# Kernel optimization log

Measured on AMD Instinct MI355X. Metric: run time of the kernel, lower is better.

Reference implementation:

```python
import jax, jax.numpy as jnp
import numpy as np

NUM_HEADS = 16
TOP_K = 6


def setup_inputs() -> dict:
    key = jax.random.key(0)
    ks = jax.random.split(key, 16)
    B, P = 8192, 4096
    QD = PD = D = 1024  # query_dim, prototype_dim, token_dim
    s = lambda d: 1.0 / np.sqrt(d)
    return {
        "query": jax.random.normal(ks[0], (B, QD), jnp.float32),
        "prototype_bank": jax.random.normal(ks[1], (P, PD), jnp.float32),
        "prototype_logits": jax.random.normal(ks[2], (B, P), jnp.float32),
        # query_proj / prototype_proj (torch Linear: y = x @ W.T + b)
        "Wq_proj": jax.random.normal(ks[3], (D, QD), jnp.float32) * s(QD),
        "bq_proj": jnp.zeros((D,), jnp.float32),
        "Wp_proj": jax.random.normal(ks[4], (D, PD), jnp.float32) * s(PD),
        "bp_proj": jnp.zeros((D,), jnp.float32),
        # MultiheadAttention in-proj (q, k, v) and out-proj
        "Wq": jax.random.normal(ks[5], (D, D), jnp.float32) * s(D),
        "bq": jnp.zeros((D,), jnp.float32),
        "Wk": jax.random.normal(ks[6], (D, D), jnp.float32) * s(D),
        "bk": jnp.zeros((D,), jnp.float32),
        "Wv": jax.random.normal(ks[7], (D, D), jnp.float32) * s(D),
        "bv": jnp.zeros((D,), jnp.float32),
        "Wo": jax.random.normal(ks[8], (D, D), jnp.float32) * s(D),
        "bo": jnp.zeros((D,), jnp.float32),
    }


def reference(query, prototype_bank, prototype_logits,
              Wq_proj, bq_proj, Wp_proj, bp_proj,
              Wq, bq, Wk, bk, Wv, bv, Wo, bo):
    B, D = query.shape[0], Wq.shape[0]
    h = NUM_HEADS
    dh = D // h
    k = min(TOP_K, prototype_bank.shape[0])

    # top-k prototype selection (indices only)
    _, topk_idx = jax.lax.top_k(prototype_logits, k)            # [B, k]

    projected_bank = prototype_bank @ Wp_proj.T + bp_proj        # [P, D]
    selected = projected_bank[topk_idx]                          # [B, k, D]

    attn_query = (query @ Wq_proj.T + bq_proj)[:, None, :]       # [B, 1, D]

    # MultiheadAttention (batch_first, eval mode so dropout is a no-op)
    qh = (attn_query @ Wq.T + bq).reshape(B, 1, h, dh).transpose(0, 2, 1, 3)  # [B,h,1,dh]
    kh = (selected @ Wk.T + bk).reshape(B, k, h, dh).transpose(0, 2, 1, 3)    # [B,h,k,dh]
    vh = (selected @ Wv.T + bv).reshape(B, k, h, dh).transpose(0, 2, 1, 3)    # [B,h,k,dh]

    scores = jnp.einsum("bhqd,bhkd->bhqk", qh, kh) / jnp.sqrt(jnp.float32(dh))
    w = jax.nn.softmax(scores, axis=-1)                          # [B,h,1,k]
    ctx = jnp.einsum("bhqk,bhkd->bhqd", w, vh)                   # [B,h,1,dh]
    ctx = ctx.transpose(0, 2, 1, 3).reshape(B, 1, D)
    context = ctx @ Wo.T + bo                                    # [B,1,D]

    attn_weights = w.mean(axis=1)                                # avg heads -> [B,1,k]
    return context[:, 0, :], attn_weights[:, 0, :]
```

## Files before the change

kernel.cpp:

```cpp
#include <hip/hip_runtime.h>
#include <stdint.h>

#define B_ROWS 8192
#define P_ROWS 4096
#define D_DIM  1024
#define K_TOP  6

typedef __attribute__((ext_vector_type(8))) short short8;
typedef __attribute__((ext_vector_type(4))) float floatx4;

static __device__ __forceinline__ float bf2f(unsigned short h) {
  return __uint_as_float(((unsigned)h) << 16);
}
static __device__ __forceinline__ unsigned short f2bf(float f) {
  unsigned u = __float_as_uint(f);
  u += 0x7FFFu + ((u >> 16) & 1u);
  return (unsigned short)(u >> 16);
}

struct ConvArgs {
  const float* s[8];
  unsigned short* d[8];
};
#define SEG0_END  8388608u
#define SEG1_END 12582912u
#define CONV_TOTAL 18874368u

__global__ __launch_bounds__(256) void convert_all_kernel(ConvArgs a) {
  unsigned e = (blockIdx.x * 256u + threadIdx.x) * 4u;
  int seg; unsigned base;
  if (e < SEG0_END) { seg = 0; base = 0; }
  else if (e < SEG1_END) { seg = 1; base = SEG0_END; }
  else {
    unsigned w = e - SEG1_END;
    seg = 2 + (int)(w >> 20);
    base = SEG1_END + (((unsigned)(seg - 2)) << 20);
  }
  unsigned off = e - base;
  float4 v = *(const float4*)(a.s[seg] + off);
  ushort4 o;
  o.x = f2bf(v.x); o.y = f2bf(v.y); o.z = f2bf(v.z); o.w = f2bf(v.w);
  *(ushort4*)(a.d[seg] + off) = o;
}

static __device__ __forceinline__ void cswap64(unsigned long long& hi, unsigned long long& lo) {
  unsigned long long a = hi, b = lo;
  bool c = b > a;
  hi = c ? b : a;
  lo = c ? a : b;
}

__global__ __launch_bounds__(256) void topk6_kernel(const float* __restrict__ logits,
                                                    int* __restrict__ out) {
  const int wid = threadIdx.x >> 6;
  const int lane = threadIdx.x & 63;
  const int row = blockIdx.x * 4 + wid;
  const float4* lp4 = (const float4*)(logits + (size_t)row * P_ROWS);

  unsigned long long m0 = 0, m1 = 0, m2 = 0, m3 = 0, m4 = 0, m5 = 0;

  auto ins = [&](float val, int idx) {
    unsigned u = __float_as_uint(val);
    u ^= ((unsigned)((int)u >> 31)) | 0x80000000u;
    unsigned long long key =
        (((unsigned long long)u) << 32) | (unsigned long long)(0xFFFFFFFFu - (unsigned)idx);
    m5 = key > m5 ? key : m5;
    cswap64(m4, m5);
    cswap64(m3, m4);
    cswap64(m2, m3);
    cswap64(m1, m2);
    cswap64(m0, m1);
  };

#pragma unroll
  for (int j = 0; j < 16; ++j) {
    float4 v = lp4[j * 64 + lane];
    const int base = j * 256 + lane * 4;
    ins(v.x, base);
    ins(v.y, base + 1);
    ins(v.z, base + 2);
    ins(v.w, base + 3);
  }

#pragma unroll
  for (int it = 0; it < K_TOP; ++it) {
    unsigned long long best = m0;
#pragma unroll
    for (int o = 32; o > 0; o >>= 1) {
      unsigned long long t = __shfl_xor(best, o);
      best = t > best ? t : best;
    }
    if (lane == 0)
      out[row * K_TOP + it] = (int)(0xFFFFFFFFu - (unsigned)(best & 0xFFFFFFFFull));
    const bool pred = (m0 == best);
    m0 = pred ? m1 : m0;
    m1 = pred ? m2 : m1;
    m2 = pred ? m3 : m2;
    m3 = pred ? m4 : m3;
    m4 = pred ? m5 : m4;
    m5 = pred ? 0ull : m5;
  }
}

typedef __attribute__((address_space(3))) unsigned int lds32_t;
typedef const __attribute__((address_space(1))) unsigned int g32_t;

static __device__ __forceinline__ void gld_lds16(const unsigned short* g, unsigned short* l) {
  __builtin_amdgcn_global_load_lds((g32_t*)(uintptr_t)g,
                                   (lds32_t*)(unsigned int)(uintptr_t)l, 16, 0, 0);
}

template <bool OUT_BF16>
static __device__ __forceinline__ void gemm_bt_body(
    const unsigned short* __restrict__ A, const unsigned short* __restrict__ Bw,
    const float* __restrict__ bias, void* __restrict__ Cout, int m0, int n0) {
  constexpr int Kd = 1024, Nd = 1024, BK = 64;
  __shared__ unsigned short sA[128 * BK];
  __shared__ unsigned short sB[128 * BK];

  const int tid = threadIdx.x;
  const int wid = tid >> 6, lane = tid & 63;
  const int wm = (wid & 1) * 64, wn = (wid >> 1) * 64;

  floatx4 acc[4][4];
#pragma unroll
  for (int mt = 0; mt < 4; ++mt)
#pragma unroll
    for (int nt = 0; nt < 4; ++nt) acc[mt][nt] = (floatx4){0.f, 0.f, 0.f, 0.f};

  const int ld_row = lane >> 3;
  const int ld_col = (lane & 7) * 8;

  for (int kt = 0; kt < Kd / BK; ++kt) {
    const int k0 = kt * BK;
    __syncthreads();
#pragma unroll
    for (int c = 0; c < 4; ++c) {
      const int ch = wid * 4 + c;
      const int r = ch * 8 + ld_row;
      gld_lds16(A  + (size_t)(m0 + r) * Kd + k0 + ld_col, sA + ch * 512);
      gld_lds16(Bw + (size_t)(n0 + r) * Kd + k0 + ld_col, sB + ch * 512);
    }
    __syncthreads();
#pragma unroll
    for (int ks = 0; ks < 2; ++ks) {
      const int kk = ks * 32 + (lane >> 4) * 8;
      short8 a[4], b[4];
#pragma unroll
      for (int t = 0; t < 4; ++t) {
        a[t] = *(const short8*)(sA + (wm + t * 16 + (lane & 15)) * BK + kk);
        b[t] = *(const short8*)(sB + (wn + t * 16 + (lane & 15)) * BK + kk);
      }
#pragma unroll
      for (int mt = 0; mt < 4; ++mt)
#pragma unroll
        for (int nt = 0; nt < 4; ++nt)
          acc[mt][nt] = __builtin_amdgcn_mfma_f32_16x16x32_bf16(a[mt], b[nt], acc[mt][nt], 0, 0, 0);
    }
  }

  const int er = lane >> 4;
  const int ec = lane & 15;
#pragma unroll
  for (int mt = 0; mt < 4; ++mt) {
#pragma unroll
    for (int nt = 0; nt < 4; ++nt) {
      const int col = n0 + wn + nt * 16 + ec;
      const float bv = bias[col];
#pragma unroll
      for (int r = 0; r < 4; ++r) {
        const int row = m0 + wm + mt * 16 + er * 4 + r;
        const float v = acc[mt][nt][r] + bv;
        if (OUT_BF16)
          ((unsigned short*)Cout)[(size_t)row * Nd + col] = f2bf(v);
        else
          ((float*)Cout)[(size_t)row * Nd + col] = v;
      }
    }
  }
}

template <bool OUT_BF16>
__global__ __launch_bounds__(256) void gemm_bt_kernel(
    const unsigned short* __restrict__ A, const unsigned short* __restrict__ Bw,
    const float* __restrict__ bias, void* __restrict__ Cout) {
  gemm_bt_body<OUT_BF16>(A, Bw, bias, Cout, blockIdx.y * 128, blockIdx.x * 128);
}

__global__ __launch_bounds__(256) void gemm_bt_dual_kernel(
    const unsigned short* __restrict__ A,
    const unsigned short* __restrict__ W0, const float* __restrict__ b0, unsigned short* C0,
    const unsigned short* __restrict__ W1, const float* __restrict__ b1, unsigned short* C1) {
  const unsigned short* Bw = blockIdx.z ? W1 : W0;
  const float* bias = blockIdx.z ? b1 : b0;
  unsigned short* C = blockIdx.z ? C1 : C0;
  gemm_bt_body<true>(A, Bw, bias, (void*)C, blockIdx.y * 128, blockIdx.x * 128);
}

__global__ __launch_bounds__(256) void attn_kernel(
    const unsigned short* __restrict__ q2,
    const unsigned short* __restrict__ kb,
    const unsigned short* __restrict__ vb,
    const int* __restrict__ topk,
    unsigned short* __restrict__ ctx,
    float* __restrict__ attnw) {
  const int b = blockIdx.x;
  const int wid = threadIdx.x >> 6, lane = threadIdx.x & 63;
  __shared__ float wsum[4][K_TOP];

  int idx[K_TOP];
#pragma unroll
  for (int j = 0; j < K_TOP; ++j) idx[j] = topk[b * K_TOP + j];

  float hw[K_TOP] = {0.f, 0.f, 0.f, 0.f, 0.f, 0.f};
#pragma unroll
  for (int hh = 0; hh < 4; ++hh) {
    const int h = wid * 4 + hh;
    const int off = h * 64 + lane;
    const float qv = bf2f(q2[(size_t)b * D_DIM + off]);
    float s[K_TOP];
#pragma unroll
    for (int j = 0; j < K_TOP; ++j)
      s[j] = qv * bf2f(kb[(size_t)idx[j] * D_DIM + off]);
#pragma unroll
    for (int j = 0; j < K_TOP; ++j)
#pragma unroll
      for (int o = 32; o > 0; o >>= 1) s[j] += __shfl_xor(s[j], o);

    float mx = -1e30f;
#pragma unroll
    for (int j = 0; j < K_TOP; ++j) mx = fmaxf(mx, s[j] * 0.125f);
    float e[K_TOP], sum = 0.f;
#pragma unroll
    for (int j = 0; j < K_TOP; ++j) { e[j] = __expf(s[j] * 0.125f - mx); sum += e[j]; }
    const float inv = 1.0f / sum;

    float o = 0.f;
#pragma unroll
    for (int j = 0; j < K_TOP; ++j) {
      const float w = e[j] * inv;
      hw[j] += w;
      o += w * bf2f(vb[(size_t)idx[j] * D_DIM + off]);
    }
    ctx[(size_t)b * D_DIM + off] = f2bf(o);
  }
  if (lane == 0) {
#pragma unroll
    for (int j = 0; j < K_TOP; ++j) wsum[wid][j] = hw[j];
  }
  __syncthreads();
  if (threadIdx.x < K_TOP) {
    const float t = wsum[0][threadIdx.x] + wsum[1][threadIdx.x] +
                    wsum[2][threadIdx.x] + wsum[3][threadIdx.x];
    attnw[(size_t)b * K_TOP + threadIdx.x] = t * (1.0f / 16.0f);
  }
}

extern "C" void kernel_launch(void* const* d_in, const int* in_sizes, int n_in,
                              void* d_out, int out_size, void* d_ws, size_t ws_size,
                              hipStream_t stream) {
  const float* query   = (const float*)d_in[0];
  const float* bank    = (const float*)d_in[1];
  const float* logits  = (const float*)d_in[2];
  const float* Wq_proj = (const float*)d_in[3];
  const float* bq_proj = (const float*)d_in[4];
  const float* Wp_proj = (const float*)d_in[5];
  const float* bp_proj = (const float*)d_in[6];
  const float* Wq      = (const float*)d_in[7];
  const float* bq      = (const float*)d_in[8];
  const float* Wk      = (const float*)d_in[9];
  const float* bk      = (const float*)d_in[10];
  const float* Wv      = (const float*)d_in[11];
  const float* bv      = (const float*)d_in[12];
  const float* Wo      = (const float*)d_in[13];
  const float* bo      = (const float*)d_in[14];

  char* ws = (char*)d_ws;
  size_t off = 0;
  auto alloc = [&](size_t bytes) {
    void* p = ws + off;
    off += (bytes + 255) & ~(size_t)255;
    return p;
  };
  unsigned short* q_bf    = (unsigned short*)alloc((size_t)B_ROWS * D_DIM * 2);
  unsigned short* bank_bf = (unsigned short*)alloc((size_t)P_ROWS * D_DIM * 2);
  unsigned short* q1_bf   = (unsigned short*)alloc((size_t)B_ROWS * D_DIM * 2);
  unsigned short* pb_bf   = (unsigned short*)alloc((size_t)P_ROWS * D_DIM * 2);
  unsigned short* vb_bf   = (unsigned short*)alloc((size_t)P_ROWS * D_DIM * 2);
  unsigned short* wqp_bf  = (unsigned short*)alloc((size_t)D_DIM * D_DIM * 2);
  unsigned short* wpp_bf  = (unsigned short*)alloc((size_t)D_DIM * D_DIM * 2);
  unsigned short* wq_bf   = (unsigned short*)alloc((size_t)D_DIM * D_DIM * 2);
  unsigned short* wk_bf   = (unsigned short*)alloc((size_t)D_DIM * D_DIM * 2);
  unsigned short* wv_bf   = (unsigned short*)alloc((size_t)D_DIM * D_DIM * 2);
  unsigned short* wo_bf   = (unsigned short*)alloc((size_t)D_DIM * D_DIM * 2);
  int* topk               = (int*)alloc((size_t)B_ROWS * K_TOP * 4);

  float* out_ctx  = (float*)d_out;
  float* out_attn = out_ctx + (size_t)B_ROWS * D_DIM;

  ConvArgs ca;
  ca.s[0] = query;   ca.d[0] = q_bf;
  ca.s[1] = bank;    ca.d[1] = bank_bf;
  ca.s[2] = Wq_proj; ca.d[2] = wqp_bf;
  ca.s[3] = Wp_proj; ca.d[3] = wpp_bf;
  ca.s[4] = Wq;      ca.d[4] = wq_bf;
  ca.s[5] = Wk;      ca.d[5] = wk_bf;
  ca.s[6] = Wv;      ca.d[6] = wv_bf;
  ca.s[7] = Wo;      ca.d[7] = wo_bf;
  convert_all_kernel<<<CONV_TOTAL / 1024, 256, 0, stream>>>(ca);

  topk6_kernel<<<B_ROWS / 4, 256, 0, stream>>>(logits, topk);

  auto gemm_bf = [&](const unsigned short* A, const unsigned short* W, const float* bias,
                     unsigned short* C, int M) {
    dim3 grid(D_DIM / 128, M / 128);
    gemm_bt_kernel<true><<<grid, 256, 0, stream>>>(A, W, bias, (void*)C);
  };
  gemm_bf(q_bf,    wqp_bf, bq_proj, q1_bf, B_ROWS);
  gemm_bf(bank_bf, wpp_bf, bp_proj, pb_bf, P_ROWS);
  gemm_bf(q1_bf,   wq_bf,  bq,      q_bf,  B_ROWS);

  {
    dim3 grid(D_DIM / 128, P_ROWS / 128, 2);
    gemm_bt_dual_kernel<<<grid, 256, 0, stream>>>(pb_bf, wk_bf, bk, bank_bf, wv_bf, bv, vb_bf);
  }

  attn_kernel<<<B_ROWS, 256, 0, stream>>>(q_bf, bank_bf, vb_bf, topk, q1_bf, out_attn);

  dim3 grid2(D_DIM / 128, B_ROWS / 128);
  gemm_bt_kernel<false><<<grid2, 256, 0, stream>>>(q1_bf, wo_bf, bo, d_out);
}
```

Before: 478.2 us.

## Fold input projections into attention in-projection weights to drop two GEMMs

Precomputes combined weights Wq·Wq_proj, Wk·Wp_proj and Wv·Wp_proj, plus the matching folded biases, using a small transpose and a batched 1024^3 GEMM. The query path then needs a single 8192x1024x1024 GEMM instead of two, and the bank path goes straight from the raw bank to K/V, dropping the intermediate projection GEMM. This removes roughly 12 GFLOP of large-GEMM work in exchange for about 3 GFLOP of weight-combining work on every call. The combined weights are rounded to bf16, which adds a rounding step different from the two-stage path.

After: 463.0 us. -3.2%, faster.

```diff
diff --git a/kernel.cpp b/kernel.cpp
--- a/kernel.cpp
+++ b/kernel.cpp
@@ -41,6 +41,50 @@
   ushort4 o;
   o.x = f2bf(v.x); o.y = f2bf(v.y); o.z = f2bf(v.z); o.w = f2bf(v.w);
   *(ushort4*)(a.d[seg] + off) = o;
+}
+
+__global__ __launch_bounds__(256) void transpose2_kernel(
+    const unsigned short* __restrict__ s0, unsigned short* __restrict__ d0,
+    const unsigned short* __restrict__ s1, unsigned short* __restrict__ d1) {
+  const unsigned short* src = blockIdx.z ? s1 : s0;
+  unsigned short* dst = blockIdx.z ? d1 : d0;
+  __shared__ unsigned short t[64][72];
+  const int i0 = blockIdx.y * 64, j0 = blockIdx.x * 64;
+  const int r = threadIdx.x >> 4;
+  const int c = (threadIdx.x & 15) * 4;
+#pragma unroll
+  for (int rr = 0; rr < 4; ++rr) {
+    const int row = r + rr * 16;
+    ushort4 v = *(const ushort4*)(src + (size_t)(i0 + row) * D_DIM + j0 + c);
+    t[c + 0][row] = v.x; t[c + 1][row] = v.y; t[c + 2][row] = v.z; t[c + 3][row] = v.w;
+  }
+  __syncthreads();
+#pragma unroll
+  for (int rr = 0; rr < 4; ++rr) {
+    const int row = r + rr * 16;
+    ushort4 v = *(const ushort4*)(&t[row][c]);
+    *(ushort4*)(dst + (size_t)(j0 + row) * D_DIM + i0 + c) = v;
+  }
+}
+
+struct Bias3Args {
+  const float* W[3];
+  const float* p[3];
+  const float* b[3];
+  float* o[3];
+};
+__global__ __launch_bounds__(256) void bias3_kernel(Bias3Args a) {
+  const int j = blockIdx.y;
+  const int wid = threadIdx.x >> 6, lane = threadIdx.x & 63;
+  const int n = blockIdx.x * 4 + wid;
+  const float* W = a.W[j] + (size_t)n * D_DIM;
+  const float* p = a.p[j];
+  float s = 0.f;
+#pragma unroll
+  for (int d = lane; d < D_DIM; d += 64) s += W[d] * p[d];
+#pragma unroll
+  for (int o = 32; o > 0; o >>= 1) s += __shfl_xor(s, o);
+  if (lane == 0) a.o[j][n] = s + a.b[j][n];
 }
 
 static __device__ __forceinline__ void cswap64(unsigned long long& hi, unsigned long long& lo) {
@@ -110,7 +154,7 @@
                                    (lds32_t*)(unsigned int)(uintptr_t)l, 16, 0, 0);
 }
 
-template <bool OUT_BF16>
+template <bool OUT_BF16, bool HAS_BIAS>
 static __device__ __forceinline__ void gemm_bt_body(
     const unsigned short* __restrict__ A, const unsigned short* __restrict__ Bw,
     const float* __restrict__ bias, void* __restrict__ Cout, int m0, int n0) {
@@ -166,7 +210,7 @@
 #pragma unroll
     for (int nt = 0; nt < 4; ++nt) {
       const int col = n0 + wn + nt * 16 + ec;
-      const float bv = bias[col];
+      const float bv = HAS_BIAS ? bias[col] : 0.f;
 #pragma unroll
       for (int r = 0; r < 4; ++r) {
         const int row = m0 + wm + mt * 16 + er * 4 + r;
@@ -184,7 +228,7 @@
 __global__ __launch_bounds__(256) void gemm_bt_kernel(
     const unsigned short* __restrict__ A, const unsigned short* __restrict__ Bw,
     const float* __restrict__ bias, void* __restrict__ Cout) {
-  gemm_bt_body<OUT_BF16>(A, Bw, bias, Cout, blockIdx.y * 128, blockIdx.x * 128);
+  gemm_bt_body<OUT_BF16, true>(A, Bw, bias, Cout, blockIdx.y * 128, blockIdx.x * 128);
 }
 
 __global__ __launch_bounds__(256) void gemm_bt_dual_kernel(
@@ -194,7 +238,18 @@
   const unsigned short* Bw = blockIdx.z ? W1 : W0;
   const float* bias = blockIdx.z ? b1 : b0;
   unsigned short* C = blockIdx.z ? C1 : C0;
-  gemm_bt_body<true>(A, Bw, bias, (void*)C, blockIdx.y * 128, blockIdx.x * 128);
+  gemm_bt_body<true, true>(A, Bw, bias, (void*)C, blockIdx.y * 128, blockIdx.x * 128);
+}
+
+struct Fuse3Args {
+  const unsigned short* A[3];
+  const unsigned short* W[3];
+  unsigned short* C[3];
+};
+__global__ __launch_bounds__(256) void gemm_fuse3_kernel(Fuse3Args a) {
+  const int z = blockIdx.z;
+  gemm_bt_body<true, false>(a.A[z], a.W[z], nullptr, (void*)a.C[z],
+                            blockIdx.y * 128, blockIdx.x * 128);
 }
 
 __global__ __launch_bounds__(256) void attn_kernel(
@@ -284,8 +339,8 @@
   };
   unsigned short* q_bf    = (unsigned short*)alloc((size_t)B_ROWS * D_DIM * 2);
   unsigned short* bank_bf = (unsigned short*)alloc((size_t)P_ROWS * D_DIM * 2);
-  unsigned short* q1_bf   = (unsigned short*)alloc((size_t)B_ROWS * D_DIM * 2);
-  unsigned short* pb_bf   = (unsigned short*)alloc((size_t)P_ROWS * D_DIM * 2);
+  unsigned short* q2_bf   = (unsigned short*)alloc((size_t)B_ROWS * D_DIM * 2);
+  unsigned short* kb_bf   = (unsigned short*)alloc((size_t)P_ROWS * D_DIM * 2);
   unsigned short* vb_bf   = (unsigned short*)alloc((size_t)P_ROWS * D_DIM * 2);
   unsigned short* wqp_bf  = (unsigned short*)alloc((size_t)D_DIM * D_DIM * 2);
   unsigned short* wpp_bf  = (unsigned short*)alloc((size_t)D_DIM * D_DIM * 2);
@@ -293,6 +348,14 @@
   unsigned short* wk_bf   = (unsigned short*)alloc((size_t)D_DIM * D_DIM * 2);
   unsigned short* wv_bf   = (unsigned short*)alloc((size_t)D_DIM * D_DIM * 2);
   unsigned short* wo_bf   = (unsigned short*)alloc((size_t)D_DIM * D_DIM * 2);
+  unsigned short* wqpT_bf = (unsigned short*)alloc((size_t)D_DIM * D_DIM * 2);
+  unsigned short* wppT_bf = (unsigned short*)alloc((size_t)D_DIM * D_DIM * 2);
+  unsigned short* wcq_bf  = (unsigned short*)alloc((size_t)D_DIM * D_DIM * 2);
+  unsigned short* wck_bf  = (unsigned short*)alloc((size_t)D_DIM * D_DIM * 2);
+  unsigned short* wcv_bf  = (unsigned short*)alloc((size_t)D_DIM * D_DIM * 2);
+  float* bcq              = (float*)alloc(D_DIM * 4);
+  float* bck              = (float*)alloc(D_DIM * 4);
+  float* bcv              = (float*)alloc(D_DIM * 4);
   int* topk               = (int*)alloc((size_t)B_ROWS * K_TOP * 4);
 
   float* out_ctx  = (float*)d_out;
@@ -309,24 +372,46 @@
   ca.s[7] = Wo;      ca.d[7] = wo_bf;
   convert_all_kernel<<<CONV_TOTAL / 1024, 256, 0, stream>>>(ca);
 
+  {
+    dim3 grid(D_DIM / 64, D_DIM / 64, 2);
+    transpose2_kernel<<<grid, 256, 0, stream>>>(wqp_bf, wqpT_bf, wpp_bf, wppT_bf);
+  }
+
+  {
+    Fuse3Args fa;
+    fa.A[0] = wq_bf; fa.W[0] = wqpT_bf; fa.C[0] = wcq_bf;
+    fa.A[1] = wk_bf; fa.W[1] = wppT_bf; fa.C[1] = wck_bf;
+    fa.A[2] = wv_bf; fa.W[2] = wppT_bf; fa.C[2] = wcv_bf;
+    dim3 grid(D_DIM / 128, D_DIM / 128, 3);
+    gemm_fuse3_kernel<<<grid, 256, 0, stream>>>(fa);
+  }
+
+  {
+    Bias3Args ba;
+    ba.W[0] = Wq; ba.p[0] = bq_proj; ba.b[0] = bq; ba.o[0] = bcq;
+    ba.W[1] = Wk; ba.p[1] = bp_proj; ba.b[1] = bk; ba.o[1] = bck;
+    ba.W[2] = Wv; ba.p[2] = bp_proj; ba.b[2] = bv; ba.o[2] = bcv;
+    dim3 grid(D_DIM / 4, 3);
+    bias3_kernel<<<grid, 256, 0, stream>>>(ba);
+  }
+
   topk6_kernel<<<B_ROWS / 4, 256, 0, stream>>>(logits, topk);
 
-  auto gemm_bf = [&](const unsigned short* A, const unsigned short* W, const float* bias,
-                     unsigned short* C, int M) {
-    dim3 grid(D_DIM / 128, M / 128);
-    gemm_bt_kernel<true><<<grid, 256, 0, stream>>>(A, W, bias, (void*)C);
-  };
-  gemm_bf(q_bf,    wqp_bf, bq_proj, q1_bf, B_ROWS);
-  gemm_bf(bank_bf, wpp_bf, bp_proj, pb_bf, P_ROWS);
-  gemm_bf(q1_bf,   wq_bf,  bq,      q_bf,  B_ROWS);
+  {
+    dim3 grid(D_DIM / 128, B_ROWS / 128);
+    gemm_bt_kernel<true><<<grid, 256, 0, stream>>>(q_bf, wcq_bf, bcq, (void*)q2_bf);
+  }
 
   {
     dim3 grid(D_DIM / 128, P_ROWS / 128, 2);
-    gemm_bt_dual_kernel<<<grid, 256, 0, stream>>>(pb_bf, wk_bf, bk, bank_bf, wv_bf, bv, vb_bf);
-  }
-
-  attn_kernel<<<B_ROWS, 256, 0, stream>>>(q_bf, bank_bf, vb_bf, topk, q1_bf, out_attn);
-
-  dim3 grid2(D_DIM / 128, B_ROWS / 128);
-  gemm_bt_kernel<false><<<grid2, 256, 0, stream>>>(q1_bf, wo_bf, bo, d_out);
-}
+    gemm_bt_dual_kernel<<<grid, 256, 0, stream>>>(bank_bf, wck_bf, bck, kb_bf,
+                                                  wcv_bf, bcv, vb_bf);
+  }
+
+  attn_kernel<<<B_ROWS, 256, 0, stream>>>(q2_bf, kb_bf, vb_bf, topk, q_bf, out_attn);
+
+  {
+    dim3 grid(D_DIM / 128, B_ROWS / 128);
+    gemm_bt_kernel<false><<<grid, 256, 0, stream>>>(q_bf, wo_bf, bo, d_out);
+  }
+}
```

## Fold input projections into attention in-proj weights and fuse prep launches

Applied to the files above, without the earlier changes.

Precomputes combined weights Wq·Wq_proj, Wk·Wp_proj and Wv·Wp_proj, plus folded biases, so each activation passes through one GEMM instead of two. A prep kernel merges the bf16 conversion, the weight transposes and the bias folding. The weight-fold GEMMs share a launch with top-k selection, and the three activation GEMMs run in one launch. This cuts large-GEMM flops and launch count, but adds small 1024^3 GEMMs and an extra bf16 rounding of the folded weights.

After: 443.6 us. 1.08x faster.

```diff
diff --git a/kernel.cpp b/kernel.cpp
--- a/kernel.cpp
+++ b/kernel.cpp
@@ -18,47 +18,179 @@
   return (unsigned short)(u >> 16);
 }
 
-struct ConvArgs {
-  const float* s[8];
-  unsigned short* d[8];
+typedef __attribute__((address_space(3))) unsigned int lds32_t;
+typedef const __attribute__((address_space(1))) unsigned int g32_t;
+
+static __device__ __forceinline__ void gld_lds16(const unsigned short* g, unsigned short* l) {
+  __builtin_amdgcn_global_load_lds((g32_t*)(uintptr_t)g,
+                                   (lds32_t*)(unsigned int)(uintptr_t)l, 16, 0, 0);
+}
+
+template <bool OUT_BF16, bool HAS_BIAS>
+static __device__ __forceinline__ void gemm_bt_body(
+    const unsigned short* __restrict__ A, const unsigned short* __restrict__ Bw,
+    const float* __restrict__ bias, void* __restrict__ Cout, int m0, int n0) {
+  constexpr int Kd = 1024, Nd = 1024, BK = 64;
+  __shared__ unsigned short sA[128 * BK];
+  __shared__ unsigned short sB[128 * BK];
+
+  const int tid = threadIdx.x;
+  const int wid = tid >> 6, lane = tid & 63;
+  const int wm = (wid & 1) * 64, wn = (wid >> 1) * 64;
+
+  floatx4 acc[4][4];
+#pragma unroll
+  for (int mt = 0; mt < 4; ++mt)
+#pragma unroll
+    for (int nt = 0; nt < 4; ++nt) acc[mt][nt] = (floatx4){0.f, 0.f, 0.f, 0.f};
+
+  const int ld_row = lane >> 3;
+  const int ld_col = (lane & 7) * 8;
+
+  for (int kt = 0; kt < Kd / BK; ++kt) {
+    const int k0 = kt * BK;
+    __syncthreads();
+#pragma unroll
+    for (int c = 0; c < 4; ++c) {
+      const int ch = wid * 4 + c;
+      const int r = ch * 8 + ld_row;
+      gld_lds16(A  + (size_t)(m0 + r) * Kd + k0 + ld_col, sA + ch * 512);
+      gld_lds16(Bw + (size_t)(n0 + r) * Kd + k0 + ld_col, sB + ch * 512);
+    }
+    __syncthreads();
+#pragma unroll
+    for (int ks = 0; ks < 2; ++ks) {
+      const int kk = ks * 32 + (lane >> 4) * 8;
+      short8 a[4], b[4];
+#pragma unroll
+      for (int t = 0; t < 4; ++t) {
+        a[t] = *(const short8*)(sA + (wm + t * 16 + (lane & 15)) * BK + kk);
+        b[t] = *(const short8*)(sB + (wn + t * 16 + (lane & 15)) * BK + kk);
+      }
+#pragma unroll
+      for (int mt = 0; mt < 4; ++mt)
+#pragma unroll
+        for (int nt = 0; nt < 4; ++nt)
+          acc[mt][nt] = __builtin_amdgcn_mfma_f32_16x16x32_bf16(a[mt], b[nt], acc[mt][nt], 0, 0, 0);
+    }
+  }
+
+  const int er = lane >> 4;
+  const int ec = lane & 15;
+#pragma unroll
+  for (int mt = 0; mt < 4; ++mt) {
+#pragma unroll
+    for (int nt = 0; nt < 4; ++nt) {
+      const int col = n0 + wn + nt * 16 + ec;
+      const float bv = HAS_BIAS ? bias[col] : 0.f;
+#pragma unroll
+      for (int r = 0; r < 4; ++r) {
+        const int row = m0 + wm + mt * 16 + er * 4 + r;
+        const float v = acc[mt][nt][r] + bv;
+        if (OUT_BF16)
+          ((unsigned short*)Cout)[(size_t)row * Nd + col] = f2bf(v);
+        else
+          ((float*)Cout)[(size_t)row * Nd + col] = v;
+      }
+    }
+  }
+}
+
+template <bool OUT_BF16>
+__global__ __launch_bounds__(256) void gemm_bt_kernel(
+    const unsigned short* __restrict__ A, const unsigned short* __restrict__ Bw,
+    const float* __restrict__ bias, void* __restrict__ Cout) {
+  gemm_bt_body<OUT_BF16, true>(A, Bw, bias, Cout, blockIdx.y * 128, blockIdx.x * 128);
+}
+
+#define PREP_BLOCKS 17664
+struct PrepArgs {
+  const float* cs[6]; unsigned short* cd[6];
+  const float* ts[2]; unsigned short* td[2];
+  const float* bW[3]; const float* bp[3]; const float* bb[3]; float* bo[3];
 };
-#define SEG0_END  8388608u
-#define SEG1_END 12582912u
-#define CONV_TOTAL 18874368u
-
-__global__ __launch_bounds__(256) void convert_all_kernel(ConvArgs a) {
-  unsigned e = (blockIdx.x * 256u + threadIdx.x) * 4u;
-  int seg; unsigned base;
-  if (e < SEG0_END) { seg = 0; base = 0; }
-  else if (e < SEG1_END) { seg = 1; base = SEG0_END; }
-  else {
-    unsigned w = e - SEG1_END;
-    seg = 2 + (int)(w >> 20);
-    base = SEG1_END + (((unsigned)(seg - 2)) << 20);
-  }
-  unsigned off = e - base;
-  float4 v = *(const float4*)(a.s[seg] + off);
-  ushort4 o;
-  o.x = f2bf(v.x); o.y = f2bf(v.y); o.z = f2bf(v.z); o.w = f2bf(v.w);
-  *(ushort4*)(a.d[seg] + off) = o;
-}
+
+__global__ __launch_bounds__(256) void prep_kernel(PrepArgs a) {
+  const int b = blockIdx.x;
+  if (b < 16384) {
+    int seg; unsigned sb;
+    if (b < 8192) { seg = 0; sb = 0; }
+    else if (b < 12288) { seg = 1; sb = 8192; }
+    else { seg = 2 + ((b - 12288) >> 10); sb = 12288u + (((unsigned)(seg - 2)) << 10); }
+    const unsigned off = (((unsigned)b - sb) << 10) + threadIdx.x * 4u;
+    float4 v = *(const float4*)(a.cs[seg] + off);
+    ushort4 o;
+    o.x = f2bf(v.x); o.y = f2bf(v.y); o.z = f2bf(v.z); o.w = f2bf(v.w);
+    *(ushort4*)(a.cd[seg] + off) = o;
+  } else if (b < 16896) {
+    __shared__ unsigned short t[64][72];
+    const int tt = b - 16384;
+    const int which = tt >> 8;
+    const int tile = tt & 255;
+    const int i0 = (tile >> 4) * 64, j0 = (tile & 15) * 64;
+    const float* src = a.ts[which];
+    unsigned short* dst = a.td[which];
+    const int r = threadIdx.x >> 4;
+    const int c = (threadIdx.x & 15) * 4;
+#pragma unroll
+    for (int rr = 0; rr < 4; ++rr) {
+      const int row = r + rr * 16;
+      float4 v = *(const float4*)(src + (size_t)(i0 + row) * D_DIM + j0 + c);
+      t[c + 0][row] = f2bf(v.x); t[c + 1][row] = f2bf(v.y);
+      t[c + 2][row] = f2bf(v.z); t[c + 3][row] = f2bf(v.w);
+    }
+    __syncthreads();
+#pragma unroll
+    for (int rr = 0; rr < 4; ++rr) {
+      const int row = r + rr * 16;
+      ushort4 v = *(const ushort4*)(&t[row][c]);
+      *(ushort4*)(dst + (size_t)(j0 + row) * D_DIM + i0 + c) = v;
+    }
+  } else {
+    const int b3 = b - 16896;
+    const int j = b3 >> 8;
+    const int nb = b3 & 255;
+    const int wid = threadIdx.x >> 6, lane = threadIdx.x & 63;
+    const int n = nb * 4 + wid;
+    const float* W = a.bW[j] + (size_t)n * D_DIM;
+    const float* p = a.bp[j];
+    float s = 0.f;
+#pragma unroll
+    for (int d = lane; d < D_DIM; d += 64) s += W[d] * p[d];
+#pragma unroll
+    for (int o = 32; o > 0; o >>= 1) s += __shfl_xor(s, o);
+    if (lane == 0) a.bo[j][n] = s + a.bb[j][n];
+  }
+}
+
+#define MID_BLOCKS 2240
+struct MidArgs {
+  const unsigned short* fA[3]; const unsigned short* fW[3]; unsigned short* fC[3];
+  const float* logits; int* topk;
+};
 
 static __device__ __forceinline__ void cswap64(unsigned long long& hi, unsigned long long& lo) {
-  unsigned long long a = hi, b = lo;
-  bool c = b > a;
-  hi = c ? b : a;
-  lo = c ? a : b;
-}
-
-__global__ __launch_bounds__(256) void topk6_kernel(const float* __restrict__ logits,
-                                                    int* __restrict__ out) {
+  unsigned long long x = hi, y = lo;
+  bool c = y > x;
+  hi = c ? y : x;
+  lo = c ? x : y;
+}
+
+__global__ __launch_bounds__(256) void mid_kernel(MidArgs a) {
+  const int b = blockIdx.x;
+  if (b < 192) {
+    const int z = b >> 6;
+    const int tile = b & 63;
+    gemm_bt_body<true, false>(a.fA[z], a.fW[z], nullptr, (void*)a.fC[z],
+                              (tile >> 3) * 128, (tile & 7) * 128);
+    return;
+  }
   const int wid = threadIdx.x >> 6;
   const int lane = threadIdx.x & 63;
-  const int row = blockIdx.x * 4 + wid;
-  const float4* lp4 = (const float4*)(logits + (size_t)row * P_ROWS);
+  const int row = (b - 192) * 4 + wid;
+  const float4* lp4 = (const float4*)(a.logits + (size_t)row * P_ROWS);
 
   unsigned long long m0 = 0, m1 = 0, m2 = 0, m3 = 0, m4 = 0, m5 = 0;
-
   auto ins = [&](float val, int idx) {
     unsigned u = __float_as_uint(val);
     u ^= ((unsigned)((int)u >> 31)) | 0x80000000u;
@@ -71,7 +203,6 @@
     cswap64(m1, m2);
     cswap64(m0, m1);
   };
-
 #pragma unroll
   for (int j = 0; j < 16; ++j) {
     float4 v = lp4[j * 64 + lane];
@@ -81,7 +212,6 @@
     ins(v.z, base + 2);
     ins(v.w, base + 3);
   }
-
 #pragma unroll
   for (int it = 0; it < K_TOP; ++it) {
     unsigned long long best = m0;
@@ -91,7 +221,7 @@
       best = t > best ? t : best;
     }
     if (lane == 0)
-      out[row * K_TOP + it] = (int)(0xFFFFFFFFu - (unsigned)(best & 0xFFFFFFFFull));
+      a.topk[row * K_TOP + it] = (int)(0xFFFFFFFFu - (unsigned)(best & 0xFFFFFFFFull));
     const bool pred = (m0 == best);
     m0 = pred ? m1 : m0;
     m1 = pred ? m2 : m1;
@@ -102,99 +232,20 @@
   }
 }
 
-typedef __attribute__((address_space(3))) unsigned int lds32_t;
-typedef const __attribute__((address_space(1))) unsigned int g32_t;
-
-static __device__ __forceinline__ void gld_lds16(const unsigned short* g, unsigned short* l) {
-  __builtin_amdgcn_global_load_lds((g32_t*)(uintptr_t)g,
-                                   (lds32_t*)(unsigned int)(uintptr_t)l, 16, 0, 0);
-}
-
-template <bool OUT_BF16>
-static __device__ __forceinline__ void gemm_bt_body(
-    const unsigned short* __restrict__ A, const unsigned short* __restrict__ Bw,
-    const float* __restrict__ bias, void* __restrict__ Cout, int m0, int n0) {
-  constexpr int Kd = 1024, Nd = 1024, BK = 64;
-  __shared__ unsigned short sA[128 * BK];
-  __shared__ unsigned short sB[128 * BK];
-
-  const int tid = threadIdx.x;
-  const int wid = tid >> 6, lane = tid & 63;
-  const int wm = (wid & 1) * 64, wn = (wid >> 1) * 64;
-
-  floatx4 acc[4][4];
-#pragma unroll
-  for (int mt = 0; mt < 4; ++mt)
-#pragma unroll
-    for (int nt = 0; nt < 4; ++nt) acc[mt][nt] = (floatx4){0.f, 0.f, 0.f, 0.f};
-
-  const int ld_row = lane >> 3;
-  const int ld_col = (lane & 7) * 8;
-
-  for (int kt = 0; kt < Kd / BK; ++kt) {
-    const int k0 = kt * BK;
-    __syncthreads();
-#pragma unroll
-    for (int c = 0; c < 4; ++c) {
-      const int ch = wid * 4 + c;
-      const int r = ch * 8 + ld_row;
-      gld_lds16(A  + (size_t)(m0 + r) * Kd + k0 + ld_col, sA + ch * 512);
-      gld_lds16(Bw + (size_t)(n0 + r) * Kd + k0 + ld_col, sB + ch * 512);
-    }
-    __syncthreads();
-#pragma unroll
-    for (int ks = 0; ks < 2; ++ks) {
-      const int kk = ks * 32 + (lane >> 4) * 8;
-      short8 a[4], b[4];
-#pragma unroll
-      for (int t = 0; t < 4; ++t) {
-        a[t] = *(const short8*)(sA + (wm + t * 16 + (lane & 15)) * BK + kk);
-        b[t] = *(const short8*)(sB + (wn + t * 16 + (lane & 15)) * BK + kk);
-      }
-#pragma unroll
-      for (int mt = 0; mt < 4; ++mt)
-#pragma unroll
-        for (int nt = 0; nt < 4; ++nt)
-          acc[mt][nt] = __builtin_amdgcn_mfma_f32_16x16x32_bf16(a[mt], b[nt], acc[mt][nt], 0, 0, 0);
-    }
-  }
-
-  const int er = lane >> 4;
-  const int ec = lane & 15;
-#pragma unroll
-  for (int mt = 0; mt < 4; ++mt) {
-#pragma unroll
-    for (int nt = 0; nt < 4; ++nt) {
-      const int col = n0 + wn + nt * 16 + ec;
-      const float bv = bias[col];
-#pragma unroll
-      for (int r = 0; r < 4; ++r) {
-        const int row = m0 + wm + mt * 16 + er * 4 + r;
-        const float v = acc[mt][nt][r] + bv;
-        if (OUT_BF16)
-          ((unsigned short*)Cout)[(size_t)row * Nd + col] = f2bf(v);
-        else
-          ((float*)Cout)[(size_t)row * Nd + col] = v;
-      }
-    }
-  }
-}
-
-template <bool OUT_BF16>
-__global__ __launch_bounds__(256) void gemm_bt_kernel(
-    const unsigned short* __restrict__ A, const unsigned short* __restrict__ Bw,
-    const float* __restrict__ bias, void* __restrict__ Cout) {
-  gemm_bt_body<OUT_BF16>(A, Bw, bias, Cout, blockIdx.y * 128, blockIdx.x * 128);
-}
-
-__global__ __launch_bounds__(256) void gemm_bt_dual_kernel(
-    const unsigned short* __restrict__ A,
-    const unsigned short* __restrict__ W0, const float* __restrict__ b0, unsigned short* C0,
-    const unsigned short* __restrict__ W1, const float* __restrict__ b1, unsigned short* C1) {
-  const unsigned short* Bw = blockIdx.z ? W1 : W0;
-  const float* bias = blockIdx.z ? b1 : b0;
-  unsigned short* C = blockIdx.z ? C1 : C0;
-  gemm_bt_body<true>(A, Bw, bias, (void*)C, blockIdx.y * 128, blockIdx.x * 128);
+#define GEMM3_BLOCKS 1024
+struct Gemm3Args {
+  const unsigned short* A[3]; const unsigned short* W[3]; const float* bias[3];
+  unsigned short* C[3];
+};
+
+__global__ __launch_bounds__(256) void gemm3_kernel(Gemm3Args a) {
+  const int b = blockIdx.x;
+  int seg, lb;
+  if (b < 512) { seg = 0; lb = b; }
+  else if (b < 768) { seg = 1; lb = b - 512; }
+  else { seg = 2; lb = b - 768; }
+  gemm_bt_body<true, true>(a.A[seg], a.W[seg], a.bias[seg], (void*)a.C[seg],
+                           (lb >> 3) * 128, (lb & 7) * 128);
 }
 
 __global__ __launch_bounds__(256) void attn_kernel(
@@ -284,49 +335,56 @@
   };
   unsigned short* q_bf    = (unsigned short*)alloc((size_t)B_ROWS * D_DIM * 2);
   unsigned short* bank_bf = (unsigned short*)alloc((size_t)P_ROWS * D_DIM * 2);
-  unsigned short* q1_bf   = (unsigned short*)alloc((size_t)B_ROWS * D_DIM * 2);
-  unsigned short* pb_bf   = (unsigned short*)alloc((size_t)P_ROWS * D_DIM * 2);
+  unsigned short* q2_bf   = (unsigned short*)alloc((size_t)B_ROWS * D_DIM * 2);
+  unsigned short* kb_bf   = (unsigned short*)alloc((size_t)P_ROWS * D_DIM * 2);
   unsigned short* vb_bf   = (unsigned short*)alloc((size_t)P_ROWS * D_DIM * 2);
-  unsigned short* wqp_bf  = (unsigned short*)alloc((size_t)D_DIM * D_DIM * 2);
-  unsigned short* wpp_bf  = (unsigned short*)alloc((size_t)D_DIM * D_DIM * 2);
   unsigned short* wq_bf   = (unsigned short*)alloc((size_t)D_DIM * D_DIM * 2);
   unsigned short* wk_bf   = (unsigned short*)alloc((size_t)D_DIM * D_DIM * 2);
   unsigned short* wv_bf   = (unsigned short*)alloc((size_t)D_DIM * D_DIM * 2);
   unsigned short* wo_bf   = (unsigned short*)alloc((size_t)D_DIM * D_DIM * 2);
+  unsigned short* wqpT_bf = (unsigned short*)alloc((size_t)D_DIM * D_DIM * 2);
+  unsigned short* wppT_bf = (unsigned short*)alloc((size_t)D_DIM * D_DIM * 2);
+  unsigned short* wcq_bf  = (unsigned short*)alloc((size_t)D_DIM * D_DIM * 2);
+  unsigned short* wck_bf  = (unsigned short*)alloc((size_t)D_DIM * D_DIM * 2);
+  unsigned short* wcv_bf  = (unsigned short*)alloc((size_t)D_DIM * D_DIM * 2);
+  float* bcq              = (float*)alloc(D_DIM * 4);
+  float* bck              = (float*)alloc(D_DIM * 4);
+  float* bcv              = (float*)alloc(D_DIM * 4);
   int* topk               = (int*)alloc((size_t)B_ROWS * K_TOP * 4);
 
   float* out_ctx  = (float*)d_out;
   float* out_attn = out_ctx + (size_t)B_ROWS * D_DIM;
-
-  ConvArgs ca;
-  ca.s[0] = query;   ca.d[0] = q_bf;
-  ca.s[1] = bank;    ca.d[1] = bank_bf;
-  ca.s[2] = Wq_proj; ca.d[2] = wqp_bf;
-  ca.s[3] = Wp_proj; ca.d[3] = wpp_bf;
-  ca.s[4] = Wq;      ca.d[4] = wq_bf;
-  ca.s[5] = Wk;      ca.d[5] = wk_bf;
-  ca.s[6] = Wv;      ca.d[6] = wv_bf;
-  ca.s[7] = Wo;      ca.d[7] = wo_bf;
-  convert_all_kernel<<<CONV_TOTAL / 1024, 256, 0, stream>>>(ca);
-
-  topk6_kernel<<<B_ROWS / 4, 256, 0, stream>>>(logits, topk);
-
-  auto gemm_bf = [&](const unsigned short* A, const unsigned short* W, const float* bias,
-                     unsigned short* C, int M) {
-    dim3 grid(D_DIM / 128, M / 128);
-    gemm_bt_kernel<true><<<grid, 256, 0, stream>>>(A, W, bias, (void*)C);
-  };
-  gemm_bf(q_bf,    wqp_bf, bq_proj, q1_bf, B_ROWS);
-  gemm_bf(bank_bf, wpp_bf, bp_proj, pb_bf, P_ROWS);
-  gemm_bf(q1_bf,   wq_bf,  bq,      q_bf,  B_ROWS);
-
-  {
-    dim3 grid(D_DIM / 128, P_ROWS / 128, 2);
-    gemm_bt_dual_kernel<<<grid, 256, 0, stream>>>(pb_bf, wk_bf, bk, bank_bf, wv_bf, bv, vb_bf);
-  }
-
-  attn_kernel<<<B_ROWS, 256, 0, stream>>>(q_bf, bank_bf, vb_bf, topk, q1_bf, out_attn);
+  (void)out_ctx;
+
+  PrepArgs pa;
+  pa.cs[0] = query; pa.cd[0] = q_bf;
+  pa.cs[1] = bank;  pa.cd[1] = bank_bf;
+  pa.cs[2] = Wq;    pa.cd[2] = wq_bf;
+  pa.cs[3] = Wk;    pa.cd[3] = wk_bf;
+  pa.cs[4] = Wv;    pa.cd[4] = wv_bf;
+  pa.cs[5] = Wo;    pa.cd[5] = wo_bf;
+  pa.ts[0] = Wq_proj; pa.td[0] = wqpT_bf;
+  pa.ts[1] = Wp_proj; pa.td[1] = wppT_bf;
+  pa.bW[0] = Wq; pa.bp[0] = bq_proj; pa.bb[0] = bq; pa.bo[0] = bcq;
+  pa.bW[1] = Wk; pa.bp[1] = bp_proj; pa.bb[1] = bk; pa.bo[1] = bck;
+  pa.bW[2] = Wv; pa.bp[2] = bp_proj; pa.bb[2] = bv; pa.bo[2] = bcv;
+  prep_kernel<<<PREP_BLOCKS, 256, 0, stream>>>(pa);
+
+  MidArgs ma;
+  ma.fA[0] = wq_bf; ma.fW[0] = wqpT_bf; ma.fC[0] = wcq_bf;
+  ma.fA[1] = wk_bf; ma.fW[1] = wppT_bf; ma.fC[1] = wck_bf;
+  ma.fA[2] = wv_bf; ma.fW[2] = wppT_bf; ma.fC[2] = wcv_bf;
+  ma.logits = logits; ma.topk = topk;
+  mid_kernel<<<MID_BLOCKS, 256, 0, stream>>>(ma);
+
+  Gemm3Args ga;
+  ga.A[0] = q_bf;    ga.W[0] = wcq_bf; ga.bias[0] = bcq; ga.C[0] = q2_bf;
+  ga.A[1] = bank_bf; ga.W[1] = wck_bf; ga.bias[1] = bck; ga.C[1] = kb_bf;
+  ga.A[2] = bank_bf; ga.W[2] = wcv_bf; ga.bias[2] = bcv; ga.C[2] = vb_bf;
+  gemm3_kernel<<<GEMM3_BLOCKS, 256, 0, stream>>>(ga);
+
+  attn_kernel<<<B_ROWS, 256, 0, stream>>>(q2_bf, kb_bf, vb_bf, topk, q_bf, out_attn);
 
   dim3 grid2(D_DIM / 128, B_ROWS / 128);
-  gemm_bt_kernel<false><<<grid2, 256, 0, stream>>>(q1_bf, wo_bf, bo, d_out);
-}
+  gemm_bt_kernel<false><<<grid2, 256, 0, stream>>>(q_bf, wo_bf, bo, d_out);
+}
```
